# Kernel optimization log

Hardware: AMD Instinct MI355X
Metric: run time of the kernel (lower is better)

Reference implementation:

```python
import jax, jax.numpy as jnp
import numpy as np

N_SRC = 1_000_000   # source neurons
E = 4_000_000       # total gathered inputs (edges)
S = 250_000         # output neurons (segments)
D = 64              # value feature dim


def setup_inputs() -> dict:
    key = jax.random.key(0)
    k1, k2, k3 = jax.random.split(key, 3)
    values = jax.random.normal(k1, (N_SRC, D), dtype=jnp.float32)
    gather_idx = jax.random.randint(k2, (E,), 0, N_SRC, dtype=jnp.int64)
    # sorted segment ids emulate the contiguous split-by-inputs_dims layout
    segment_ids = jnp.sort(jax.random.randint(k3, (E,), 0, S, dtype=jnp.int64))
    return {
        "values": values,
        "gather_idx": gather_idx,
        "segment_ids": segment_ids,
        "num_segments": S,
    }


def reference(values, gather_idx, segment_ids, num_segments):
    # gather scattered neuron values (equivalent of self.gather(layer_values))
    gathered = values[gather_idx]  # [E, D]
    # ragged segmented sum (equivalent of split + pad_sequence + sum over dim=1)
    sums = jax.ops.segment_sum(gathered, segment_ids, num_segments=num_segments)  # [S, D]
    # mean: divide by per-segment input counts (inputs_dims_tensor)
    counts = jax.ops.segment_sum(
        jnp.ones((gathered.shape[0],), dtype=gathered.dtype),
        segment_ids,
        num_segments=num_segments,
    )
    counts = jnp.maximum(counts, 1.0)  # guard empty segments (original always has >=1 input)
    return sums / counts[:, None]
```

## Files before the change

### kernel.cpp

```cpp
#include <hip/hip_runtime.h>

__global__ __launch_bounds__(256) void build_rowptr_kernel(
    const int* __restrict__ segid, int* __restrict__ rowptr, int E, int S)
{
    const int e = blockIdx.x * blockDim.x + threadIdx.x;
    if (e >= E) return;
    const int cur  = segid[e];
    const int prev = (e == 0) ? -1 : segid[e - 1];
    for (int s = prev + 1; s <= cur; ++s) rowptr[s] = e;
    if (e == E - 1) {
        for (int s = cur + 1; s <= S; ++s) rowptr[s] = E;
    }
}

__global__ __launch_bounds__(256) void seg_mean_kernel(
    const float4* __restrict__ values4,
    const int*    __restrict__ gidx,
    const int*    __restrict__ rowptr,
    float4*       __restrict__ out4,
    int S)
{
    const int wave = (blockIdx.x * blockDim.x + threadIdx.x) >> 6;
    if (wave >= S) return;
    const int lane = threadIdx.x & 63;
    const int g = lane >> 4;
    const int f = lane & 15;

    const int start = rowptr[wave];
    const int end   = rowptr[wave + 1];
    const int cnt   = end - start;

    float sx = 0.f, sy = 0.f, sz = 0.f, sw = 0.f;

    for (int base = 0; base < cnt; base += 64) {
        const int nq = min(64, cnt - base);
        const int p  = start + base + lane;
        int myidx = (p < end) ? gidx[p] : 0;
        const int iters = (nq + 3) >> 2;
        #pragma unroll 4
        for (int it = 0; it < iters; ++it) {
            const int e   = (it << 2) + g;
            const int idx = __shfl(myidx, e);
            if (e < nq) {
                const float4 v = values4[(size_t)idx * 16 + f];
                sx += v.x; sy += v.y; sz += v.z; sw += v.w;
            }
        }
    }

    sx += __shfl_xor(sx, 16); sy += __shfl_xor(sy, 16);
    sz += __shfl_xor(sz, 16); sw += __shfl_xor(sw, 16);
    sx += __shfl_xor(sx, 32); sy += __shfl_xor(sy, 32);
    sz += __shfl_xor(sz, 32); sw += __shfl_xor(sw, 32);

    if (lane < 16) {
        const float inv = 1.0f / (float)(cnt > 0 ? cnt : 1);
        float4 o;
        o.x = sx * inv; o.y = sy * inv; o.z = sz * inv; o.w = sw * inv;
        out4[(size_t)wave * 16 + f] = o;
    }
}

extern "C" void kernel_launch(void* const* d_in, const int* in_sizes, int n_in,
                              void* d_out, int out_size, void* d_ws, size_t ws_size,
                              hipStream_t stream) {
    const float4* values4 = (const float4*)d_in[0];
    const int*    gidx    = (const int*)d_in[1];
    const int*    segid   = (const int*)d_in[2];
    float4* out4   = (float4*)d_out;
    int*    rowptr = (int*)d_ws;

    const int E = in_sizes[1];
    const int S = out_size / 64;

    build_rowptr_kernel<<<(E + 255) / 256, 256, 0, stream>>>(segid, rowptr, E, S);

    const int threads = 256;
    const int grid = (S + 3) / 4;
    seg_mean_kernel<<<grid, threads, 0, stream>>>(values4, gidx, rowptr, out4, S);
}
```

Before: 167.4 us.

## Map each 16-lane quarter-wave to its own segment instead of one segment per wave

Each wavefront now handles four segments, one per 16-lane group, rather than splitting one segment's edges across four groups. This removes the cross-group shuffle reduction and cuts the number of waves by four, but segments with different edge counts inside one wave now diverge. The early exit happens per lane before a shuffle, so a partially active last wave could read from inactive lanes, though only its own group's lanes are read. Gathered rows are still 256-byte float4 loads per edge.

```diff
diff --git a/kernel.cpp b/kernel.cpp
--- a/kernel.cpp
+++ b/kernel.cpp
@@ -21,44 +21,36 @@
     int S)
 {
     const int wave = (blockIdx.x * blockDim.x + threadIdx.x) >> 6;
-    if (wave >= S) return;
     const int lane = threadIdx.x & 63;
-    const int g = lane >> 4;
-    const int f = lane & 15;
+    const int g    = lane >> 4;
+    const int f    = lane & 15;
+    const int sg   = (wave << 2) + g;
+    if (sg >= S) return;
 
-    const int start = rowptr[wave];
-    const int end   = rowptr[wave + 1];
+    const int start = rowptr[sg];
+    const int end   = rowptr[sg + 1];
     const int cnt   = end - start;
 
-    float sx = 0.f, sy = 0.f, sz = 0.f, sw = 0.f;
+    float ax = 0.f, ay = 0.f, az = 0.f, aw = 0.f;
 
-    for (int base = 0; base < cnt; base += 64) {
-        const int nq = min(64, cnt - base);
-        const int p  = start + base + lane;
-        int myidx = (p < end) ? gidx[p] : 0;
-        const int iters = (nq + 3) >> 2;
-        #pragma unroll 4
-        for (int it = 0; it < iters; ++it) {
-            const int e   = (it << 2) + g;
-            const int idx = __shfl(myidx, e);
-            if (e < nq) {
+    for (int base = 0; base < cnt; base += 16) {
+        const int p     = start + base + f;
+        const int myidx = (p < end) ? gidx[p] : 0;
+        const int n     = min(16, cnt - base);
+        #pragma unroll 8
+        for (int it = 0; it < 16; ++it) {
+            if (it < n) {
+                const int idx = __shfl(myidx, (g << 4) | it);
                 const float4 v = values4[(size_t)idx * 16 + f];
-                sx += v.x; sy += v.y; sz += v.z; sw += v.w;
+                ax += v.x; ay += v.y; az += v.z; aw += v.w;
             }
         }
     }
 
-    sx += __shfl_xor(sx, 16); sy += __shfl_xor(sy, 16);
-    sz += __shfl_xor(sz, 16); sw += __shfl_xor(sw, 16);
-    sx += __shfl_xor(sx, 32); sy += __shfl_xor(sy, 32);
-    sz += __shfl_xor(sz, 32); sw += __shfl_xor(sw, 32);
-
-    if (lane < 16) {
-        const float inv = 1.0f / (float)(cnt > 0 ? cnt : 1);
-        float4 o;
-        o.x = sx * inv; o.y = sy * inv; o.z = sz * inv; o.w = sw * inv;
-        out4[(size_t)wave * 16 + f] = o;
-    }
+    const float inv = 1.0f / (float)(cnt > 0 ? cnt : 1);
+    float4 o;
+    o.x = ax * inv; o.y = ay * inv; o.z = az * inv; o.w = aw * inv;
+    out4[(size_t)sg * 16 + f] = o;
 }
 
 extern "C" void kernel_launch(void* const* d_in, const int* in_sizes, int n_in,
@@ -75,7 +67,9 @@
 
     build_rowptr_kernel<<<(E + 255) / 256, 256, 0, stream>>>(segid, rowptr, E, S);
 
-    const int threads = 256;
-    const int grid = (S + 3) / 4;
-    seg_mean_kernel<<<grid, threads, 0, stream>>>(values4, gidx, rowptr, out4, S);
+    const int segsPerWave  = 4;
+    const int wavesNeeded  = (S + segsPerWave - 1) / segsPerWave;
+    const int threads      = 256;
+    const int blocks       = (wavesNeeded * 64 + threads - 1) / threads;
+    seg_mean_kernel<<<blocks, threads, 0, stream>>>(values4, gidx, rowptr, out4, S);
 }
```

Measured after the change: 170.2 us. About the same (+1.7%).
